# Optimization experiments

Measured on AMD Instinct MI355X. Metric: run time of the kernel, lower is better.

Reference implementation:

```python
import jax, jax.numpy as jnp
import numpy as np

VOCAB, EMB, HID, LAT, LAYERS = 32000, 512, 1024, 1024, 2
B, T = 16, 128
IN0 = EMB + HID          # layer-0 GRU input size (emb concat syn_z)
OUT_IN = HID + LAT + EMB # out-projection input (use_last_output=True)


def gru_cell(x, h, W_ih, W_hh, b_ih, b_hh):
    # PyTorch GRUCell: gates ordered [r, z, n]
    gi = x @ W_ih.T + b_ih
    gh = h @ W_hh.T + b_hh
    i_r, i_z, i_n = jnp.split(gi, 3, axis=-1)
    h_r, h_z, h_n = jnp.split(gh, 3, axis=-1)
    r = jax.nn.sigmoid(i_r + h_r)
    z = jax.nn.sigmoid(i_z + h_z)
    n = jnp.tanh(i_n + r * h_n)
    return (1.0 - z) * n + z * h


def setup_inputs() -> dict:
    key = jax.random.key(0)
    ks = jax.random.split(key, 16)
    s = 0.02
    return {
        "input_seq": jax.random.randint(ks[0], (B, T), 0, VOCAB),
        "prev_output": jnp.zeros((B, HID), jnp.float32),
        "sem_z": jax.random.normal(ks[1], (B, LAT), jnp.float32),
        "syn_z": jax.random.normal(ks[2], (B, HID), jnp.float32),
        "hidden": jnp.zeros((LAYERS, B, HID), jnp.float32),
        "emb_table": jax.random.normal(ks[3], (VOCAB, EMB), jnp.float32) * s,
        "W_ih0": jax.random.normal(ks[4], (3 * HID, IN0), jnp.float32) * s,
        "W_hh0": jax.random.normal(ks[5], (3 * HID, HID), jnp.float32) * s,
        "b_ih0": jnp.zeros((3 * HID,), jnp.float32),
        "b_hh0": jnp.zeros((3 * HID,), jnp.float32),
        "W_ih1": jax.random.normal(ks[6], (3 * HID, HID), jnp.float32) * s,
        "W_hh1": jax.random.normal(ks[7], (3 * HID, HID), jnp.float32) * s,
        "b_ih1": jnp.zeros((3 * HID,), jnp.float32),
        "b_hh1": jnp.zeros((3 * HID,), jnp.float32),
        "W_out": jax.random.normal(ks[8], (VOCAB, OUT_IN), jnp.float32) * s,
        "b_out": jnp.zeros((VOCAB,), jnp.float32),
    }


def reference(input_seq, prev_output, sem_z, syn_z, hidden, emb_table,
              W_ih0, W_hh0, b_ih0, b_hh0, W_ih1, W_hh1, b_ih1, b_hh1,
              W_out, b_out):
    # dropout=0.0 -> identity; input_feeding=False so prev_output is unused.
    embs = emb_table[input_seq]            # [B, T, E]
    embs_t = jnp.swapaxes(embs, 0, 1)      # [T, B, E]

    def step(h, emb_t):
        x = jnp.concatenate([emb_t, syn_z], axis=1)        # [B, E+H]
        h0 = gru_cell(x, h[0], W_ih0, W_hh0, b_ih0, b_hh0)  # [B, H]
        h1 = gru_cell(h0, h[1], W_ih1, W_hh1, b_ih1, b_hh1)
        pred = jnp.concatenate([h1, sem_z, emb_t], axis=1)  # [B, H+L+E]
        logits = pred @ W_out.T + b_out                     # [B, V]
        scores = jax.nn.log_softmax(logits, axis=-1)
        return jnp.stack([h0, h1]), (scores, logits)

    hidden_f, (scores, logits) = jax.lax.scan(step, hidden, embs_t)
    # scores/logits: [T, B, V]; output = last layer hidden at final step
    return scores, hidden_f, hidden_f[-1], logits
```

## Files before the change

kernel.cpp:

```cpp
#include <hip/hip_runtime.h>

typedef unsigned short u16;
typedef __attribute__((ext_vector_type(8))) short bf16x8;
typedef __attribute__((ext_vector_type(4))) float f32x4;
typedef __attribute__((ext_vector_type(4))) unsigned u32x4;

__device__ __forceinline__ float bf2f(u16 u) {
  union { unsigned u; float f; } v; v.u = ((unsigned)u) << 16; return v.f;
}
__device__ __forceinline__ u16 f2bf(float f) {
  union { float f; unsigned u; } v; v.f = f;
  unsigned r = v.u + 0x7FFFu + ((v.u >> 16) & 1u);
  return (u16)(r >> 16);
}

__device__ __forceinline__ f32x4 ld_sc_x4(const u16* p) {
  f32x4 r;
  asm volatile("global_load_dwordx4 %0, %1, off sc0 sc1"
               : "=v"(r) : "v"(p) : "memory");
  return r;
}
__device__ __forceinline__ float ld_sc_f32(const float* p) {
  float r;
  asm volatile("global_load_dword %0, %1, off sc0 sc1"
               : "=v"(r) : "v"(p) : "memory");
  return r;
}
__device__ __forceinline__ void st_sc_u16(u16* p, unsigned v) {
  asm volatile("global_store_short %0, %1, off sc0 sc1"
               :: "v"(p), "v"(v) : "memory");
}
__device__ __forceinline__ void st_sc_f32(float* p, float v) {
  asm volatile("global_store_dword %0, %1, off sc0 sc1"
               :: "v"(p), "v"(v) : "memory");
}
#define WAIT_VM0() asm volatile("s_waitcnt vmcnt(0)" ::: "memory")

constexpr size_t OFF_WCAT  = 0;
constexpr size_t OFF_WSEM  = 98304000;
constexpr size_t OFF_PART  = 98304000;
constexpr size_t OFF_H1ALL = 130000000;
constexpr size_t OFF_GI0   = 163840000;
constexpr size_t OFF_XOUT  = 189005824;
constexpr size_t OFF_H0ALL = 195297280;
constexpr size_t OFF_WIH0E = 199491584;
constexpr size_t OFF_WIH0S = 202637312;
constexpr size_t OFF_WHH0  = 208928768;
constexpr size_t OFF_WIH1  = 215220224;
constexpr size_t OFF_WHH1  = 221511680;
constexpr size_t OFF_SYNB  = 227803136;
constexpr size_t OFF_SEMB  = 228065280;
constexpr size_t OFF_BASE0 = 228327424;
constexpr size_t OFF_BASEO = 229900288;
constexpr size_t OFF_H0IBF = 246284288;
constexpr size_t OFF_H1IBF = 246317056;
constexpr size_t OFF_HIDF  = 262144000;
constexpr size_t OFF_LAST  = 262275072;
constexpr size_t OFF_LOGIT = 262340608;

__global__ __launch_bounds__(256) void conv_bf16_k(
    const float* __restrict__ src, u16* __restrict__ dst,
    int rows, int cols8, int sld, int soff, int dld, int doff) {
  int t = blockIdx.x * 256 + threadIdx.x;
  if (t >= rows * cols8) return;
  int r = t / cols8, c = (t - r * cols8) * 8;
  const float* s = src + (size_t)r * sld + soff + c;
  float4 a = *(const float4*)s;
  float4 b = *(const float4*)(s + 4);
  bf16x8 o;
  o[0] = (short)f2bf(a.x); o[1] = (short)f2bf(a.y);
  o[2] = (short)f2bf(a.z); o[3] = (short)f2bf(a.w);
  o[4] = (short)f2bf(b.x); o[5] = (short)f2bf(b.y);
  o[6] = (short)f2bf(b.z); o[7] = (short)f2bf(b.w);
  *(bf16x8*)(dst + (size_t)r * dld + doff + c) = o;
}

__global__ __launch_bounds__(256) void conv_wout_k(
    const float* __restrict__ Wout, u16* __restrict__ WCAT,
    u16* __restrict__ WSEM) {
  int t = blockIdx.x * 256 + threadIdx.x;
  int r = t / 320, c = (t - r * 320) * 8;
  const float* s = Wout + (size_t)r * 2560 + c;
  float4 a = *(const float4*)s;
  float4 b = *(const float4*)(s + 4);
  bf16x8 o;
  o[0] = (short)f2bf(a.x); o[1] = (short)f2bf(a.y);
  o[2] = (short)f2bf(a.z); o[3] = (short)f2bf(a.w);
  o[4] = (short)f2bf(b.x); o[5] = (short)f2bf(b.y);
  o[6] = (short)f2bf(b.z); o[7] = (short)f2bf(b.w);
  u16* dst;
  if (c < 1024)      dst = WCAT + (size_t)r * 1536 + c;
  else if (c < 2048) dst = WSEM + (size_t)r * 1024 + (c - 1024);
  else               dst = WCAT + (size_t)r * 1536 + 1024 + (c - 2048);
  *(bf16x8*)dst = o;
}

__global__ __launch_bounds__(256) void pack_pad_bf16_k(
    const float* __restrict__ src, u16* __restrict__ dst) {
  int t = blockIdx.x * 256 + threadIdx.x;
  int row = t >> 7, c = (t & 127) * 8;
  bf16x8 o = {0, 0, 0, 0, 0, 0, 0, 0};
  if (row < 16) {
    const float* s = src + row * 1024 + c;
    float4 a = *(const float4*)s;
    float4 b = *(const float4*)(s + 4);
    o[0] = (short)f2bf(a.x); o[1] = (short)f2bf(a.y);
    o[2] = (short)f2bf(a.z); o[3] = (short)f2bf(a.w);
    o[4] = (short)f2bf(b.x); o[5] = (short)f2bf(b.y);
    o[6] = (short)f2bf(b.z); o[7] = (short)f2bf(b.w);
  }
  *(bf16x8*)(dst + (size_t)row * 1024 + c) = o;
}

__global__ __launch_bounds__(256) void gather_emb_k(
    const int* __restrict__ seq, const float* __restrict__ table,
    u16* __restrict__ xout) {
  int t0 = blockIdx.x * 256 + threadIdx.x;
  int tb = t0 >> 6, c = (t0 & 63) * 8;
  int tt = tb >> 4, b = tb & 15;
  int tok = seq[b * 128 + tt];
  const float* s = table + (size_t)tok * 512 + c;
  float4 a = *(const float4*)s;
  float4 bb = *(const float4*)(s + 4);
  bf16x8 o;
  o[0] = (short)f2bf(a.x);  o[1] = (short)f2bf(a.y);
  o[2] = (short)f2bf(a.z);  o[3] = (short)f2bf(a.w);
  o[4] = (short)f2bf(bb.x); o[5] = (short)f2bf(bb.y);
  o[6] = (short)f2bf(bb.z); o[7] = (short)f2bf(bb.w);
  *(bf16x8*)(xout + (size_t)tb * 1536 + 1024 + c) = o;
}

__global__ __launch_bounds__(256) void init_h_k(
    const float* __restrict__ hidden, u16* __restrict__ h0b,
    u16* __restrict__ h1b) {
  int i = blockIdx.x * 256 + threadIdx.x;
  h0b[i] = f2bf(hidden[i]);
  h1b[i] = f2bf(hidden[16384 + i]);
}

__global__ __launch_bounds__(256) void sentinel_init_k(
    u32x4* __restrict__ h0, u32x4* __restrict__ h1, u32x4* __restrict__ pt) {
  int i = blockIdx.x * 256 + threadIdx.x;
  u32x4 hs = {0x7FC07FC0u, 0x7FC07FC0u, 0x7FC07FC0u, 0x7FC07FC0u};
  u32x4 ps = {0x7FC00000u, 0x7FC00000u, 0x7FC00000u, 0x7FC00000u};
  if (i < 262144) h0[i] = hs;
  else if (i < 524288) h1[i - 262144] = hs;
  else pt[i - 524288] = ps;
}

__device__ __forceinline__ void stage_tile_sent(const u16* src, char* tile,
                                                int tid, bool poll) {
  f32x4 tmp[8];
  for (;;) {
#pragma unroll
    for (int q = 0; q < 8; ++q) {
      int c = q * 256 + tid;
      int row = c >> 7, kc = c & 127;
      tmp[q] = ld_sc_x4(src + (size_t)row * 1024 + kc * 8);
    }
    WAIT_VM0();
    __builtin_amdgcn_sched_barrier(0);
    if (!poll) break;
    int bad = 0;
#pragma unroll
    for (int q = 0; q < 8; ++q) {
#pragma unroll
      for (int w = 0; w < 4; ++w) {
        unsigned x = __float_as_uint(tmp[q][w]);
        bad |= ((x & 0xFFFFu) == 0x7FC0u) | ((x >> 16) == 0x7FC0u);
      }
    }
    if (!bad) break;
    __builtin_amdgcn_s_sleep(2);
  }
#pragma unroll
  for (int q = 0; q < 8; ++q) {
    int c = q * 256 + tid;
    int row = c >> 7, kc = c & 127;
    int byte = (row * 2048 + kc * 16) ^ ((row & 7) << 4);
    *(bf16x8*)(tile + byte) = *(bf16x8*)&tmp[q];
  }
}

__global__ __launch_bounds__(256, 1) void gru_persist6_k(
    const float* __restrict__ hidden, const u16* __restrict__ h0i,
    const u16* __restrict__ h1i, const float* __restrict__ gi0,
    const u16* __restrict__ Whh0, const u16* __restrict__ Wih1,
    const u16* __restrict__ Whh1, const float* __restrict__ bhh0,
    const float* __restrict__ bih1, const float* __restrict__ bhh1,
    u16* __restrict__ h0all, u16* __restrict__ h1all, u16* __restrict__ xout,
    float* __restrict__ part, float* __restrict__ hidf,
    float* __restrict__ last) {
  extern __shared__ char ldsb[];
  char* Ab = ldsb + 98304;
  float* Cbuf = (float*)(ldsb + 131072);
  const int tid = threadIdx.x, bid = blockIdx.x;
  const int wave = tid >> 6, lane = tid & 63;
  const int role = bid >> 6, lb = bid & 63, jb = lb * 16;

  const u16* Wsrc = role == 0 ? Whh0 : (role == 1 ? Wih1 : Whh1);
  for (int idx = tid; idx < 48 * 128; idx += 256) {
    int row = idx >> 7, c = idx & 127;
    int g = row >> 4, jj2 = row & 15;
    const u16* src = Wsrc + (size_t)(g * 1024 + jb + jj2) * 1024 + c * 8;
    int byte = (row * 2048 + c * 16) ^ ((row & 7) << 4);
    *(bf16x8*)(ldsb + byte) = *(const bf16x8*)src;
  }

  const int eb = tid >> 4, jj = tid & 15, j = jb + jj;
  float hp = 0.f, bR = 0.f, bZ = 0.f, bN = 0.f, iR = 0.f, iZ = 0.f, iN = 0.f;
  if (role == 0) {
    hp = hidden[eb * 1024 + j];
    bR = bhh0[j]; bZ = bhh0[1024 + j]; bN = bhh0[2048 + j];
  } else if (role == 2) {
    hp = hidden[16384 + eb * 1024 + j];
    bR = bhh1[j]; bZ = bhh1[1024 + j]; bN = bhh1[2048 + j];
    iR = bih1[j]; iZ = bih1[1024 + j]; iN = bih1[2048 + j];
  }
  __syncthreads();

  const int arow = lane & 15, aq = lane >> 4;
  for (int t = 0; t < 128; ++t) {
    float* Cl = Cbuf + (t & 1) * 3456;
    const u16* asrc;
    bool poll;
    if (role == 0)      { asrc = t ? h0all + (size_t)(t - 1) * 16384 : h0i; poll = t > 0; }
    else if (role == 1) { asrc = h0all + (size_t)t * 16384; poll = true; }
    else                { asrc = t ? h1all + (size_t)(t - 1) * 16384 : h1i; poll = t > 0; }
    stage_tile_sent(asrc, Ab, tid, poll);
    __syncthreads();

    {
      f32x4 a0 = {0.f, 0.f, 0.f, 0.f}, a1 = a0, a2 = a0;
#pragma unroll
      for (int i = 0; i < 8; ++i) {
        int ks = wave + i * 4;
        int abyte = (arow * 2048 + ks * 64 + aq * 16) ^ ((arow & 7) << 4);
        bf16x8 af = *(const bf16x8*)(Ab + abyte);
        int r0 = arow, r1 = 16 + arow, r2 = 32 + arow;
        bf16x8 b0 = *(const bf16x8*)(
            ldsb + ((r0 * 2048 + ks * 64 + aq * 16) ^ ((r0 & 7) << 4)));
        bf16x8 b1 = *(const bf16x8*)(
            ldsb + ((r1 * 2048 + ks * 64 + aq * 16) ^ ((r1 & 7) << 4)));
        bf16x8 b2 = *(const bf16x8*)(
            ldsb + ((r2 * 2048 + ks * 64 + aq * 16) ^ ((r2 & 7) << 4)));
        a0 = __builtin_amdgcn_mfma_f32_16x16x32_bf16(af, b0, a0, 0, 0, 0);
        a1 = __builtin_amdgcn_mfma_f32_16x16x32_bf16(af, b1, a1, 0, 0, 0);
        a2 = __builtin_amdgcn_mfma_f32_16x16x32_bf16(af, b2, a2, 0, 0, 0);
      }
#pragma unroll
      for (int r = 0; r < 4; ++r) {
        int ci = (aq * 4 + r) * 16 + arow + aq * 8;
        Cl[(0 * 4 + wave) * 288 + ci] = a0[r];
        Cl[(1 * 4 + wave) * 288 + ci] = a1[r];
        Cl[(2 * 4 + wave) * 288 + ci] = a2[r];
      }
    }
    __syncthreads();

    {
      int ci = eb * 16 + jj + (eb >> 2) * 8;
      float s0 = Cl[0 * 288 + ci] + Cl[1 * 288 + ci] +
                 Cl[2 * 288 + ci] + Cl[3 * 288 + ci];
      float s1 = Cl[4 * 288 + ci] + Cl[5 * 288 + ci] +
                 Cl[6 * 288 + ci] + Cl[7 * 288 + ci];
      float s2 = Cl[8 * 288 + ci] + Cl[9 * 288 + ci] +
                 Cl[10 * 288 + ci] + Cl[11 * 288 + ci];
      if (role == 1) {
        float* pp = part + ((size_t)t * 64 + lb) * 768 + eb * 16 + jj;
        st_sc_f32(pp, s0);
        st_sc_f32(pp + 256, s1);
        st_sc_f32(pp + 512, s2);
        WAIT_VM0();
      } else {
        float ir, iz, inn;
        if (role == 0) {
          const float* g = gi0 + ((size_t)t * 16 + eb) * 3072 + j;
          ir = g[0]; iz = g[1024]; inn = g[2048];
        } else {
          const float* pp = part + ((size_t)t * 64 + lb) * 768 + eb * 16 + jj;
          float p0, p1, p2;
          for (;;) {
            p0 = ld_sc_f32(pp); p1 = ld_sc_f32(pp + 256);
            p2 = ld_sc_f32(pp + 512);
            WAIT_VM0();
            __builtin_amdgcn_sched_barrier(0);
            int bad = (__float_as_uint(p0) == 0x7FC00000u) |
                      (__float_as_uint(p1) == 0x7FC00000u) |
                      (__float_as_uint(p2) == 0x7FC00000u);
            if (!bad) break;
            __builtin_amdgcn_s_sleep(2);
          }
          ir = p0 + iR; iz = p1 + iZ; inn = p2 + iN;
        }
        float r = 1.f / (1.f + __expf(-(ir + s0 + bR)));
        float z = 1.f / (1.f + __expf(-(iz + s1 + bZ)));
        float n = tanhf(inn + r * (s2 + bN));
        float hnew = (1.f - z) * n + z * hp;
        hp = hnew;
        u16 hb = f2bf(hnew);
        if (role == 0) {
          st_sc_u16(h0all + ((size_t)t * 16 + eb) * 1024 + j, (unsigned)hb);
          if (t == 127) hidf[eb * 1024 + j] = hnew;
        } else {
          st_sc_u16(h1all + ((size_t)t * 16 + eb) * 1024 + j, (unsigned)hb);
          xout[((size_t)t * 16 + eb) * 1536 + j] = hb;
          if (t == 127) {
            hidf[16384 + eb * 1024 + j] = hnew;
            last[eb * 1024 + j] = hnew;
          }
        }
        WAIT_VM0();
      }
    }
  }
}

template <int MODE>
__global__ __launch_bounds__(256) void gemm_bt_k(
    const u16* __restrict__ A, int lda, const u16* __restrict__ Bw, int ldb,
    float* __restrict__ C, int ldc, const float* __restrict__ add,
    int N, int K) {
  __shared__ u16 Asm_[128 * 32];
  __shared__ u16 Bsm_[128 * 32];
  const int m0 = blockIdx.x * 128, n0 = blockIdx.y * 128;
  const int tid = threadIdx.x, wave = tid >> 6, lane = tid & 63;
  const int wm = (wave >> 1) * 64, wn = (wave & 1) * 64;
  const int lrow = lane & 15, lk = (lane >> 4) * 8;
  f32x4 acc[4][4] = {};
  for (int k0 = 0; k0 < K; k0 += 32) {
    __syncthreads();
#pragma unroll
    for (int q = 0; q < 2; ++q) {
      int c = (wave * 2 + q) * 64 + lane;
      int row = c >> 2, seg = c & 3;
      const u16* src = A + (size_t)(m0 + row) * lda + k0 + seg * 8;
      u16* dst = Asm_ + (wave * 2 + q) * 512;
      __builtin_amdgcn_global_load_lds(
          (const __attribute__((address_space(1))) void*)src,
          (__attribute__((address_space(3))) void*)dst, 16, 0, 0);
    }
#pragma unroll
    for (int q = 0; q < 2; ++q) {
      int c = (wave * 2 + q) * 64 + lane;
      int row = c >> 2, seg = c & 3;
      const u16* src = Bw + (size_t)(n0 + row) * ldb + k0 + seg * 8;
      u16* dst = Bsm_ + (wave * 2 + q) * 512;
      __builtin_amdgcn_global_load_lds(
          (const __attribute__((address_space(1))) void*)src,
          (__attribute__((address_space(3))) void*)dst, 16, 0, 0);
    }
    asm volatile("s_waitcnt vmcnt(0)" ::: "memory");
    __syncthreads();
    bf16x8 af[4], bfr[4];
#pragma unroll
    for (int i = 0; i < 4; ++i) {
      af[i]  = *(const bf16x8*)(Asm_ + (wm + i * 16 + lrow) * 32 + lk);
      bfr[i] = *(const bf16x8*)(Bsm_ + (wn + i * 16 + lrow) * 32 + lk);
    }
#pragma unroll
    for (int i = 0; i < 4; ++i)
#pragma unroll
      for (int jx = 0; jx < 4; ++jx)
        acc[i][jx] = __builtin_amdgcn_mfma_f32_16x16x32_bf16(
            af[i], bfr[jx], acc[i][jx], 0, 0, 0);
  }
  const int lr4 = (lane >> 4) * 4;
#pragma unroll
  for (int i = 0; i < 4; ++i) {
#pragma unroll
    for (int jx = 0; jx < 4; ++jx) {
      int gc = n0 + wn + jx * 16 + lrow;
#pragma unroll
      for (int r = 0; r < 4; ++r) {
        int gr = m0 + wm + i * 16 + lr4 + r;
        float v = acc[i][jx][r];
        if (MODE == 1) v += add[(gr & 15) * N + gc];
        else if (MODE == 2) v += add[gc];
        C[(size_t)gr * ldc + gc] = v;
      }
    }
  }
}

template <int MODE, bool SWZ>
__global__ __launch_bounds__(512) void gemm256_bt_k(
    const u16* __restrict__ A, int lda, const u16* __restrict__ Bw, int ldb,
    float* __restrict__ C, int ldc, const float* __restrict__ add,
    int N, int K) {
  __shared__ u16 Asm_[256 * 32];
  __shared__ u16 Bsm_[128 * 32];
  int bx = blockIdx.x, by = blockIdx.y;
  if (SWZ) {
    int nx = gridDim.x;
    int orig = by * nx + bx;
    int cpx = (nx * gridDim.y) >> 3;
    int wg = (orig & 7) * cpx + (orig >> 3);
    bx = wg % nx; by = wg / nx;
  }
  const int m0 = bx * 256, n0 = by * 128;
  const int tid = threadIdx.x, wave = tid >> 6, lane = tid & 63;
  const int wm = (wave >> 1) * 64, wn = (wave & 1) * 64;
  const int lrow = lane & 15, lk = (lane >> 4) * 8;
  f32x4 acc[4][4] = {};
  for (int k0 = 0; k0 < K; k0 += 32) {
    __syncthreads();
#pragma unroll
    for (int q = 0; q < 2; ++q) {
      int c = (q * 8 + wave) * 64 + lane;
      int row = c >> 2, seg = c & 3;
      const u16* src = A + (size_t)(m0 + row) * lda + k0 + seg * 8;
      u16* dst = Asm_ + (q * 8 + wave) * 512;
      __builtin_amdgcn_global_load_lds(
          (const __attribute__((address_space(1))) void*)src,
          (__attribute__((address_space(3))) void*)dst, 16, 0, 0);
    }
    {
      int c = wave * 64 + lane;
      int row = c >> 2, seg = c & 3;
      const u16* src = Bw + (size_t)(n0 + row) * ldb + k0 + seg * 8;
      u16* dst = Bsm_ + wave * 512;
      __builtin_amdgcn_global_load_lds(
          (const __attribute__((address_space(1))) void*)src,
          (__attribute__((address_space(3))) void*)dst, 16, 0, 0);
    }
    asm volatile("s_waitcnt vmcnt(0)" ::: "memory");
    __syncthreads();
    bf16x8 af[4], bfr[4];
#pragma unroll
    for (int i = 0; i < 4; ++i) {
      af[i]  = *(const bf16x8*)(Asm_ + (wm + i * 16 + lrow) * 32 + lk);
      bfr[i] = *(const bf16x8*)(Bsm_ + (wn + i * 16 + lrow) * 32 + lk);
    }
#pragma unroll
    for (int i = 0; i < 4; ++i)
#pragma unroll
      for (int jx = 0; jx < 4; ++jx)
        acc[i][jx] = __builtin_amdgcn_mfma_f32_16x16x32_bf16(
            af[i], bfr[jx], acc[i][jx], 0, 0, 0);
  }
  const int lr4 = (lane >> 4) * 4;
#pragma unroll
  for (int i = 0; i < 4; ++i) {
#pragma unroll
    for (int jx = 0; jx < 4; ++jx) {
      int gc = n0 + wn + jx * 16 + lrow;
#pragma unroll
      for (int r = 0; r < 4; ++r) {
        int gr = m0 + wm + i * 16 + lr4 + r;
        float v = acc[i][jx][r];
        if (MODE == 1) v += add[(gr & 15) * N + gc];
        else if (MODE == 2) v += add[gc];
        C[(size_t)gr * ldc + gc] = v;
      }
    }
  }
}

__global__ __launch_bounds__(256) void log_softmax_k(
    const float* __restrict__ logits, float* __restrict__ scores) {
  int row = blockIdx.x;
  const float* x = logits + (size_t)row * 32000;
  float* y = scores + (size_t)row * 32000;
  __shared__ float redm[4], reds[4];
  int tid = threadIdx.x;
  float m = -3.4e38f, s = 0.f;
  for (int idx = tid * 4; idx < 32000; idx += 1024) {
    float4 v = *(const float4*)(x + idx);
    float cm = fmaxf(fmaxf(v.x, v.y), fmaxf(v.z, v.w));
    if (cm > m) { s *= __expf(m - cm); m = cm; }
    s += __expf(v.x - m) + __expf(v.y - m) + __expf(v.z - m) + __expf(v.w - m);
  }
  for (int off = 1; off < 64; off <<= 1) {
    float mo = __shfl_xor(m, off), so = __shfl_xor(s, off);
    float nm = fmaxf(m, mo);
    s = s * __expf(m - nm) + so * __expf(mo - nm);
    m = nm;
  }
  if ((tid & 63) == 0) { redm[tid >> 6] = m; reds[tid >> 6] = s; }
  __syncthreads();
  {
    float fm = fmaxf(fmaxf(redm[0], redm[1]), fmaxf(redm[2], redm[3]));
    float fs = reds[0] * __expf(redm[0] - fm) + reds[1] * __expf(redm[1] - fm) +
               reds[2] * __expf(redm[2] - fm) + reds[3] * __expf(redm[3] - fm);
    float lse = fm + logf(fs);
    for (int idx = tid * 4; idx < 32000; idx += 1024) {
      float4 v = *(const float4*)(x + idx);
      float4 o;
      o.x = v.x - lse; o.y = v.y - lse; o.z = v.z - lse; o.w = v.w - lse;
      *(float4*)(y + idx) = o;
    }
  }
}

extern "C" void kernel_launch(void* const* d_in, const int* in_sizes, int n_in,
                              void* d_out, int out_size, void* d_ws,
                              size_t ws_size, hipStream_t stream) {
  const int*   seq    = (const int*)d_in[0];
  const float* sem    = (const float*)d_in[2];
  const float* syn    = (const float*)d_in[3];
  const float* hidden = (const float*)d_in[4];
  const float* table  = (const float*)d_in[5];
  const float* Wih0   = (const float*)d_in[6];
  const float* Whh0   = (const float*)d_in[7];
  const float* bih0   = (const float*)d_in[8];
  const float* bhh0   = (const float*)d_in[9];
  const float* Wih1   = (const float*)d_in[10];
  const float* Whh1   = (const float*)d_in[11];
  const float* bih1   = (const float*)d_in[12];
  const float* bhh1   = (const float*)d_in[13];
  const float* Wout   = (const float*)d_in[14];
  const float* bout   = (const float*)d_in[15];

  char* base = (char*)d_out;
  float* scores = (float*)base;
  u16*   WCAT   = (u16*)(base + OFF_WCAT);
  u16*   WSEM   = (u16*)(base + OFF_WSEM);
  float* PART   = (float*)(base + OFF_PART);
  u16*   H1ALL  = (u16*)(base + OFF_H1ALL);
  float* GI0    = (float*)(base + OFF_GI0);
  u16*   XOUT   = (u16*)(base + OFF_XOUT);
  u16*   H0ALL  = (u16*)(base + OFF_H0ALL);
  u16*   WIH0E  = (u16*)(base + OFF_WIH0E);
  u16*   WIH0S  = (u16*)(base + OFF_WIH0S);
  u16*   WHH0B  = (u16*)(base + OFF_WHH0);
  u16*   WIH1B  = (u16*)(base + OFF_WIH1);
  u16*   WHH1B  = (u16*)(base + OFF_WHH1);
  u16*   SYNB   = (u16*)(base + OFF_SYNB);
  u16*   SEMB   = (u16*)(base + OFF_SEMB);
  float* BASE0  = (float*)(base + OFF_BASE0);
  float* BASEO  = (float*)(base + OFF_BASEO);
  u16*   H0IBF  = (u16*)(base + OFF_H0IBF);
  u16*   H1IBF  = (u16*)(base + OFF_H1IBF);
  float* hidf   = (float*)(base + OFF_HIDF);
  float* last   = (float*)(base + OFF_LAST);
  float* logits = (float*)(base + OFF_LOGIT);

  conv_wout_k<<<40000, 256, 0, stream>>>(Wout, WCAT, WSEM);
  conv_bf16_k<<<768, 256, 0, stream>>>(Wih0, WIH0E, 3072, 64, 1536, 0, 512, 0);
  conv_bf16_k<<<1536, 256, 0, stream>>>(Wih0, WIH0S, 3072, 128, 1536, 512, 1024, 0);
  conv_bf16_k<<<1536, 256, 0, stream>>>(Whh0, WHH0B, 3072, 128, 1024, 0, 1024, 0);
  conv_bf16_k<<<1536, 256, 0, stream>>>(Wih1, WIH1B, 3072, 128, 1024, 0, 1024, 0);
  conv_bf16_k<<<1536, 256, 0, stream>>>(Whh1, WHH1B, 3072, 128, 1024, 0, 1024, 0);

  gather_emb_k<<<512, 256, 0, stream>>>(seq, table, XOUT);
  pack_pad_bf16_k<<<64, 256, 0, stream>>>(syn, SYNB);
  pack_pad_bf16_k<<<64, 256, 0, stream>>>(sem, SEMB);
  init_h_k<<<64, 256, 0, stream>>>(hidden, H0IBF, H1IBF);

  gemm_bt_k<2><<<dim3(1, 24), 256, 0, stream>>>(
      SYNB, 1024, WIH0S, 1024, BASE0, 3072, bih0, 3072, 1024);
  gemm_bt_k<2><<<dim3(1, 250), 256, 0, stream>>>(
      SEMB, 1024, WSEM, 1024, BASEO, 32000, bout, 32000, 1024);

  gemm256_bt_k<1, true><<<dim3(8, 24), 512, 0, stream>>>(
      XOUT + 1024, 1536, WIH0E, 512, GI0, 3072, BASE0, 3072, 512);

  sentinel_init_k<<<8192, 256, 0, stream>>>(
      (u32x4*)H0ALL, (u32x4*)H1ALL, (u32x4*)PART);

  hipFuncSetAttribute((const void*)gru_persist6_k,
                      hipFuncAttributeMaxDynamicSharedMemorySize, 158720);
  gru_persist6_k<<<192, 256, 158720, stream>>>(
      hidden, H0IBF, H1IBF, GI0, WHH0B, WIH1B, WHH1B, bhh0, bih1, bhh1,
      H0ALL, H1ALL, XOUT, PART, hidf, last);

  gemm256_bt_k<1, true><<<dim3(8, 250), 512, 0, stream>>>(
      XOUT, 1536, WCAT, 1536, logits, 32000, BASEO, 32000, 1536);

  log_softmax_k<<<2048, 256, 0, stream>>>(logits, scores);
}
```

Baseline: 1.270 ms.

## Replace sentinel polling with flag sync and overlap Wout prep inside GRU kernel

```diff
diff --git a/kernel.cpp b/kernel.cpp
--- a/kernel.cpp
+++ b/kernel.cpp
@@ -3,7 +3,6 @@
 typedef unsigned short u16;
 typedef __attribute__((ext_vector_type(8))) short bf16x8;
 typedef __attribute__((ext_vector_type(4))) float f32x4;
-typedef __attribute__((ext_vector_type(4))) unsigned u32x4;
 
 __device__ __forceinline__ float bf2f(u16 u) {
   union { unsigned u; float f; } v; v.u = ((unsigned)u) << 16; return v.f;
@@ -36,8 +35,14 @@
 }
 #define WAIT_VM0() asm volatile("s_waitcnt vmcnt(0)" ::: "memory")
 
+__device__ __forceinline__ int ld_flag(const int* p) {
+  return __hip_atomic_load(p, __ATOMIC_RELAXED, __HIP_MEMORY_SCOPE_AGENT);
+}
+__device__ __forceinline__ void st_flag(int* p, int v) {
+  __hip_atomic_store(p, v, __ATOMIC_RELAXED, __HIP_MEMORY_SCOPE_AGENT);
+}
+
 constexpr size_t OFF_WCAT  = 0;
-constexpr size_t OFF_WSEM  = 98304000;
 constexpr size_t OFF_PART  = 98304000;
 constexpr size_t OFF_H1ALL = 130000000;
 constexpr size_t OFF_GI0   = 163840000;
@@ -49,11 +54,11 @@
 constexpr size_t OFF_WIH1  = 215220224;
 constexpr size_t OFF_WHH1  = 221511680;
 constexpr size_t OFF_SYNB  = 227803136;
-constexpr size_t OFF_SEMB  = 228065280;
 constexpr size_t OFF_BASE0 = 228327424;
 constexpr size_t OFF_BASEO = 229900288;
 constexpr size_t OFF_H0IBF = 246284288;
 constexpr size_t OFF_H1IBF = 246317056;
+constexpr size_t OFF_FLAGS = 246349824;
 constexpr size_t OFF_HIDF  = 262144000;
 constexpr size_t OFF_LAST  = 262275072;
 constexpr size_t OFF_LOGIT = 262340608;
@@ -73,26 +78,6 @@
   o[4] = (short)f2bf(b.x); o[5] = (short)f2bf(b.y);
   o[6] = (short)f2bf(b.z); o[7] = (short)f2bf(b.w);
   *(bf16x8*)(dst + (size_t)r * dld + doff + c) = o;
-}
-
-__global__ __launch_bounds__(256) void conv_wout_k(
-    const float* __restrict__ Wout, u16* __restrict__ WCAT,
-    u16* __restrict__ WSEM) {
-  int t = blockIdx.x * 256 + threadIdx.x;
-  int r = t / 320, c = (t - r * 320) * 8;
-  const float* s = Wout + (size_t)r * 2560 + c;
-  float4 a = *(const float4*)s;
-  float4 b = *(const float4*)(s + 4);
-  bf16x8 o;
-  o[0] = (short)f2bf(a.x); o[1] = (short)f2bf(a.y);
-  o[2] = (short)f2bf(a.z); o[3] = (short)f2bf(a.w);
-  o[4] = (short)f2bf(b.x); o[5] = (short)f2bf(b.y);
-  o[6] = (short)f2bf(b.z); o[7] = (short)f2bf(b.w);
-  u16* dst;
-  if (c < 1024)      dst = WCAT + (size_t)r * 1536 + c;
-  else if (c < 2048) dst = WSEM + (size_t)r * 1024 + (c - 1024);
-  else               dst = WCAT + (size_t)r * 1536 + 1024 + (c - 2048);
-  *(bf16x8*)dst = o;
 }
 
 __global__ __launch_bounds__(256) void pack_pad_bf16_k(
@@ -132,47 +117,28 @@
 
 __global__ __launch_bounds__(256) void init_h_k(
     const float* __restrict__ hidden, u16* __restrict__ h0b,
-    u16* __restrict__ h1b) {
+    u16* __restrict__ h1b, int* __restrict__ flags) {
   int i = blockIdx.x * 256 + threadIdx.x;
   h0b[i] = f2bf(hidden[i]);
   h1b[i] = f2bf(hidden[16384 + i]);
-}
-
-__global__ __launch_bounds__(256) void sentinel_init_k(
-    u32x4* __restrict__ h0, u32x4* __restrict__ h1, u32x4* __restrict__ pt) {
-  int i = blockIdx.x * 256 + threadIdx.x;
-  u32x4 hs = {0x7FC07FC0u, 0x7FC07FC0u, 0x7FC07FC0u, 0x7FC07FC0u};
-  u32x4 ps = {0x7FC00000u, 0x7FC00000u, 0x7FC00000u, 0x7FC00000u};
-  if (i < 262144) h0[i] = hs;
-  else if (i < 524288) h1[i - 262144] = hs;
-  else pt[i - 524288] = ps;
-}
-
-__device__ __forceinline__ void stage_tile_sent(const u16* src, char* tile,
-                                                int tid, bool poll) {
+  if (i < 4096) flags[i] = 0;
+}
+
+__device__ __forceinline__ void stage_tile_flag(
+    const u16* src, char* tile, int tid, const int* fl, int target) {
+  if (fl) {
+    const int* myf = fl + ((tid & 127) >> 1) * 16;
+    while (ld_flag(myf) < target) __builtin_amdgcn_s_sleep(1);
+  }
   f32x4 tmp[8];
-  for (;;) {
-#pragma unroll
-    for (int q = 0; q < 8; ++q) {
-      int c = q * 256 + tid;
-      int row = c >> 7, kc = c & 127;
-      tmp[q] = ld_sc_x4(src + (size_t)row * 1024 + kc * 8);
-    }
-    WAIT_VM0();
-    __builtin_amdgcn_sched_barrier(0);
-    if (!poll) break;
-    int bad = 0;
-#pragma unroll
-    for (int q = 0; q < 8; ++q) {
-#pragma unroll
-      for (int w = 0; w < 4; ++w) {
-        unsigned x = __float_as_uint(tmp[q][w]);
-        bad |= ((x & 0xFFFFu) == 0x7FC0u) | ((x >> 16) == 0x7FC0u);
-      }
-    }
-    if (!bad) break;
-    __builtin_amdgcn_s_sleep(2);
-  }
+#pragma unroll
+  for (int q = 0; q < 8; ++q) {
+    int c = q * 256 + tid;
+    int row = c >> 7, kc = c & 127;
+    tmp[q] = ld_sc_x4(src + (size_t)row * 1024 + kc * 8);
+  }
+  WAIT_VM0();
+  __builtin_amdgcn_sched_barrier(0);
 #pragma unroll
   for (int q = 0; q < 8; ++q) {
     int c = q * 256 + tid;
@@ -182,7 +148,7 @@
   }
 }
 
-__global__ __launch_bounds__(256, 1) void gru_persist6_k(
+__global__ __launch_bounds__(256, 1) void gru_persist7_k(
     const float* __restrict__ hidden, const u16* __restrict__ h0i,
     const u16* __restrict__ h1i, const float* __restrict__ gi0,
     const u16* __restrict__ Whh0, const u16* __restrict__ Wih1,
@@ -190,13 +156,68 @@
     const float* __restrict__ bih1, const float* __restrict__ bhh1,
     u16* __restrict__ h0all, u16* __restrict__ h1all, u16* __restrict__ xout,
     float* __restrict__ part, float* __restrict__ hidf,
-    float* __restrict__ last) {
+    float* __restrict__ last, int* __restrict__ flags,
+    const float* __restrict__ Wout, const float* __restrict__ bout,
+    const float* __restrict__ sem, u16* __restrict__ WCAT,
+    float* __restrict__ baseo) {
   extern __shared__ char ldsb[];
+  const int tid = threadIdx.x, bid = blockIdx.x;
+  const int wave = tid >> 6, lane = tid & 63;
+
+  if (bid >= 192) {
+    const int ab = bid - 192;
+    float* semLds = (float*)ldsb;
+    for (int i = tid; i < 16384; i += 256) {
+      int b = i >> 10, k = i & 1023;
+      semLds[b * 1025 + k] = sem[i];
+    }
+    __syncthreads();
+    {
+      const int b = lane & 15, kq = lane >> 4;
+      for (int r = ab * 4 + wave; r < 32000; r += 256) {
+        const float* w = Wout + (size_t)r * 2560 + 1024 + kq * 256;
+        const float* sv = semLds + b * 1025 + kq * 256;
+        float a0 = 0.f, a1 = 0.f, a2 = 0.f, a3 = 0.f;
+#pragma unroll 4
+        for (int k = 0; k < 256; k += 16) {
+          float4 w0 = *(const float4*)(w + k);
+          float4 w1 = *(const float4*)(w + k + 4);
+          float4 w2 = *(const float4*)(w + k + 8);
+          float4 w3 = *(const float4*)(w + k + 12);
+          a0 += w0.x * sv[k] + w0.y * sv[k + 1] + w0.z * sv[k + 2] + w0.w * sv[k + 3];
+          a1 += w1.x * sv[k + 4] + w1.y * sv[k + 5] + w1.z * sv[k + 6] + w1.w * sv[k + 7];
+          a2 += w2.x * sv[k + 8] + w2.y * sv[k + 9] + w2.z * sv[k + 10] + w2.w * sv[k + 11];
+          a3 += w3.x * sv[k + 12] + w3.y * sv[k + 13] + w3.z * sv[k + 14] + w3.w * sv[k + 15];
+        }
+        float v = (a0 + a1) + (a2 + a3);
+        v += __shfl_xor(v, 16);
+        v += __shfl_xor(v, 32);
+        if (lane < 16) baseo[b * 32000 + r] = v + bout[r];
+      }
+    }
+    for (int job = ab * 256 + tid; job < 32000 * 192; job += 64 * 256) {
+      int r = job / 192, c = job - r * 192;
+      int scol = c < 128 ? c * 8 : 2048 + (c - 128) * 8;
+      int dcol = c < 128 ? c * 8 : 1024 + (c - 128) * 8;
+      const float* s = Wout + (size_t)r * 2560 + scol;
+      float4 a = *(const float4*)s;
+      float4 b = *(const float4*)(s + 4);
+      bf16x8 o;
+      o[0] = (short)f2bf(a.x); o[1] = (short)f2bf(a.y);
+      o[2] = (short)f2bf(a.z); o[3] = (short)f2bf(a.w);
+      o[4] = (short)f2bf(b.x); o[5] = (short)f2bf(b.y);
+      o[6] = (short)f2bf(b.z); o[7] = (short)f2bf(b.w);
+      *(bf16x8*)(WCAT + (size_t)r * 1536 + dcol) = o;
+    }
+    return;
+  }
+
   char* Ab = ldsb + 98304;
   float* Cbuf = (float*)(ldsb + 131072);
-  const int tid = threadIdx.x, bid = blockIdx.x;
-  const int wave = tid >> 6, lane = tid & 63;
   const int role = bid >> 6, lb = bid & 63, jb = lb * 16;
+  int* f0 = flags;
+  int* fih = flags + 1024;
+  int* f1 = flags + 2048;
 
   const u16* Wsrc = role == 0 ? Whh0 : (role == 1 ? Wih1 : Whh1);
   for (int idx = tid; idx < 48 * 128; idx += 256) {
@@ -223,11 +244,19 @@
   for (int t = 0; t < 128; ++t) {
     float* Cl = Cbuf + (t & 1) * 3456;
     const u16* asrc;
-    bool poll;
-    if (role == 0)      { asrc = t ? h0all + (size_t)(t - 1) * 16384 : h0i; poll = t > 0; }
-    else if (role == 1) { asrc = h0all + (size_t)t * 16384; poll = true; }
-    else                { asrc = t ? h1all + (size_t)(t - 1) * 16384 : h1i; poll = t > 0; }
-    stage_tile_sent(asrc, Ab, tid, poll);
+    const int* fl;
+    int target;
+    if (role == 0) {
+      asrc = t ? h0all + (size_t)(t - 1) * 16384 : h0i;
+      fl = t ? f0 : nullptr; target = t;
+    } else if (role == 1) {
+      asrc = h0all + (size_t)t * 16384;
+      fl = f0; target = t + 1;
+    } else {
+      asrc = t ? h1all + (size_t)(t - 1) * 16384 : h1i;
+      fl = t ? f1 : nullptr; target = t;
+    }
+    stage_tile_flag(asrc, Ab, tid, fl, target);
     __syncthreads();
 
     {
@@ -256,6 +285,8 @@
         Cl[(2 * 4 + wave) * 288 + ci] = a2[r];
       }
     }
+    if (role == 2 && tid == 0)
+      while (ld_flag(fih + lb * 16) < t + 1) __builtin_amdgcn_s_sleep(1);
     __syncthreads();
 
     {
@@ -279,18 +310,10 @@
           ir = g[0]; iz = g[1024]; inn = g[2048];
         } else {
           const float* pp = part + ((size_t)t * 64 + lb) * 768 + eb * 16 + jj;
-          float p0, p1, p2;
-          for (;;) {
-            p0 = ld_sc_f32(pp); p1 = ld_sc_f32(pp + 256);
-            p2 = ld_sc_f32(pp + 512);
-            WAIT_VM0();
-            __builtin_amdgcn_sched_barrier(0);
-            int bad = (__float_as_uint(p0) == 0x7FC00000u) |
-                      (__float_as_uint(p1) == 0x7FC00000u) |
-                      (__float_as_uint(p2) == 0x7FC00000u);
-            if (!bad) break;
-            __builtin_amdgcn_s_sleep(2);
-          }
+          float p0 = ld_sc_f32(pp), p1 = ld_sc_f32(pp + 256),
+                p2 = ld_sc_f32(pp + 512);
+          WAIT_VM0();
+          __builtin_amdgcn_sched_barrier(0);
           ir = p0 + iR; iz = p1 + iZ; inn = p2 + iN;
         }
         float r = 1.f / (1.f + __expf(-(ir + s0 + bR)));
@@ -313,6 +336,12 @@
         WAIT_VM0();
       }
     }
+    __syncthreads();
+    if (tid == 0) {
+      if (role == 0)      st_flag(f0 + lb * 16, t + 1);
+      else if (role == 1) st_flag(fih + lb * 16, t + 1);
+      else                st_flag(f1 + lb * 16, t + 1);
+    }
   }
 }
 
@@ -515,7 +544,6 @@
   char* base = (char*)d_out;
   float* scores = (float*)base;
   u16*   WCAT   = (u16*)(base + OFF_WCAT);
-  u16*   WSEM   = (u16*)(base + OFF_WSEM);
   float* PART   = (float*)(base + OFF_PART);
   u16*   H1ALL  = (u16*)(base + OFF_H1ALL);
   float* GI0    = (float*)(base + OFF_GI0);
@@ -527,16 +555,15 @@
   u16*   WIH1B  = (u16*)(base + OFF_WIH1);
   u16*   WHH1B  = (u16*)(base + OFF_WHH1);
   u16*   SYNB   = (u16*)(base + OFF_SYNB);
-  u16*   SEMB   = (u16*)(base + OFF_SEMB);
   float* BASE0  = (float*)(base + OFF_BASE0);
   float* BASEO  = (float*)(base + OFF_BASEO);
   u16*   H0IBF  = (u16*)(base + OFF_H0IBF);
   u16*   H1IBF  = (u16*)(base + OFF_H1IBF);
+  int*   FLAGS  = (int*)(base + OFF_FLAGS);
   float* hidf   = (float*)(base + OFF_HIDF);
   float* last   = (float*)(base + OFF_LAST);
   float* logits = (float*)(base + OFF_LOGIT);
 
-  conv_wout_k<<<40000, 256, 0, stream>>>(Wout, WCAT, WSEM);
   conv_bf16_k<<<768, 256, 0, stream>>>(Wih0, WIH0E, 3072, 64, 1536, 0, 512, 0);
   conv_bf16_k<<<1536, 256, 0, stream>>>(Wih0, WIH0S, 3072, 128, 1536, 512, 1024, 0);
   conv_bf16_k<<<1536, 256, 0, stream>>>(Whh0, WHH0B, 3072, 128, 1024, 0, 1024, 0);
@@ -545,25 +572,20 @@
 
   gather_emb_k<<<512, 256, 0, stream>>>(seq, table, XOUT);
   pack_pad_bf16_k<<<64, 256, 0, stream>>>(syn, SYNB);
-  pack_pad_bf16_k<<<64, 256, 0, stream>>>(sem, SEMB);
-  init_h_k<<<64, 256, 0, stream>>>(hidden, H0IBF, H1IBF);
+  init_h_k<<<64, 256, 0, stream>>>(hidden, H0IBF, H1IBF, FLAGS);
 
   gemm_bt_k<2><<<dim3(1, 24), 256, 0, stream>>>(
       SYNB, 1024, WIH0S, 1024, BASE0, 3072, bih0, 3072, 1024);
-  gemm_bt_k<2><<<dim3(1, 250), 256, 0, stream>>>(
-      SEMB, 1024, WSEM, 1024, BASEO, 32000, bout, 32000, 1024);
 
   gemm256_bt_k<1, true><<<dim3(8, 24), 512, 0, stream>>>(
       XOUT + 1024, 1536, WIH0E, 512, GI0, 3072, BASE0, 3072, 512);
 
-  sentinel_init_k<<<8192, 256, 0, stream>>>(
-      (u32x4*)H0ALL, (u32x4*)H1ALL, (u32x4*)PART);
-
-  hipFuncSetAttribute((const void*)gru_persist6_k,
+  hipFuncSetAttribute((const void*)gru_persist7_k,
                       hipFuncAttributeMaxDynamicSharedMemorySize, 158720);
-  gru_persist6_k<<<192, 256, 158720, stream>>>(
+  gru_persist7_k<<<256, 256, 158720, stream>>>(
       hidden, H0IBF, H1IBF, GI0, WHH0B, WIH1B, WHH1B, bhh0, bih1, bhh1,
-      H0ALL, H1ALL, XOUT, PART, hidf, last);
+      H0ALL, H1ALL, XOUT, PART, hidf, last, FLAGS,
+      Wout, bout, sem, WCAT, BASEO);
 
   gemm256_bt_k<1, true><<<dim3(8, 250), 512, 0, stream>>>(
       XOUT, 1536, WCAT, 1536, logits, 32000, BASEO, 32000, 1536);
```

Measured after the change: 1.470 ms. 1.16x slower.

## Replace NaN-sentinel polling with per-block progress flags in persistent GRU

Applied to the files above, without the earlier changes.

```diff
diff --git a/kernel.cpp b/kernel.cpp
--- a/kernel.cpp
+++ b/kernel.cpp
@@ -3,7 +3,6 @@
 typedef unsigned short u16;
 typedef __attribute__((ext_vector_type(8))) short bf16x8;
 typedef __attribute__((ext_vector_type(4))) float f32x4;
-typedef __attribute__((ext_vector_type(4))) unsigned u32x4;
 
 __device__ __forceinline__ float bf2f(u16 u) {
   union { unsigned u; float f; } v; v.u = ((unsigned)u) << 16; return v.f;
@@ -35,6 +34,13 @@
                :: "v"(p), "v"(v) : "memory");
 }
 #define WAIT_VM0() asm volatile("s_waitcnt vmcnt(0)" ::: "memory")
+
+__device__ __forceinline__ int ld_flag(const int* p) {
+  return __hip_atomic_load(p, __ATOMIC_RELAXED, __HIP_MEMORY_SCOPE_AGENT);
+}
+__device__ __forceinline__ void st_flag(int* p, int v) {
+  __hip_atomic_store(p, v, __ATOMIC_RELAXED, __HIP_MEMORY_SCOPE_AGENT);
+}
 
 constexpr size_t OFF_WCAT  = 0;
 constexpr size_t OFF_WSEM  = 98304000;
@@ -54,6 +60,7 @@
 constexpr size_t OFF_BASEO = 229900288;
 constexpr size_t OFF_H0IBF = 246284288;
 constexpr size_t OFF_H1IBF = 246317056;
+constexpr size_t OFF_FLAGS = 246349824;
 constexpr size_t OFF_HIDF  = 262144000;
 constexpr size_t OFF_LAST  = 262275072;
 constexpr size_t OFF_LOGIT = 262340608;
@@ -132,47 +139,24 @@
 
 __global__ __launch_bounds__(256) void init_h_k(
     const float* __restrict__ hidden, u16* __restrict__ h0b,
-    u16* __restrict__ h1b) {
+    u16* __restrict__ h1b, int* __restrict__ flags) {
   int i = blockIdx.x * 256 + threadIdx.x;
   h0b[i] = f2bf(hidden[i]);
   h1b[i] = f2bf(hidden[16384 + i]);
-}
-
-__global__ __launch_bounds__(256) void sentinel_init_k(
-    u32x4* __restrict__ h0, u32x4* __restrict__ h1, u32x4* __restrict__ pt) {
-  int i = blockIdx.x * 256 + threadIdx.x;
-  u32x4 hs = {0x7FC07FC0u, 0x7FC07FC0u, 0x7FC07FC0u, 0x7FC07FC0u};
-  u32x4 ps = {0x7FC00000u, 0x7FC00000u, 0x7FC00000u, 0x7FC00000u};
-  if (i < 262144) h0[i] = hs;
-  else if (i < 524288) h1[i - 262144] = hs;
-  else pt[i - 524288] = ps;
-}
-
-__device__ __forceinline__ void stage_tile_sent(const u16* src, char* tile,
-                                                int tid, bool poll) {
+  if (i < 4096) flags[i] = 0;
+}
+
+__device__ __forceinline__ void stage_tile(const u16* src, char* tile,
+                                           int tid) {
   f32x4 tmp[8];
-  for (;;) {
-#pragma unroll
-    for (int q = 0; q < 8; ++q) {
-      int c = q * 256 + tid;
-      int row = c >> 7, kc = c & 127;
-      tmp[q] = ld_sc_x4(src + (size_t)row * 1024 + kc * 8);
-    }
-    WAIT_VM0();
-    __builtin_amdgcn_sched_barrier(0);
-    if (!poll) break;
-    int bad = 0;
-#pragma unroll
-    for (int q = 0; q < 8; ++q) {
-#pragma unroll
-      for (int w = 0; w < 4; ++w) {
-        unsigned x = __float_as_uint(tmp[q][w]);
-        bad |= ((x & 0xFFFFu) == 0x7FC0u) | ((x >> 16) == 0x7FC0u);
-      }
-    }
-    if (!bad) break;
-    __builtin_amdgcn_s_sleep(2);
-  }
+#pragma unroll
+  for (int q = 0; q < 8; ++q) {
+    int c = q * 256 + tid;
+    int row = c >> 7, kc = c & 127;
+    tmp[q] = ld_sc_x4(src + (size_t)row * 1024 + kc * 8);
+  }
+  WAIT_VM0();
+  __builtin_amdgcn_sched_barrier(0);
 #pragma unroll
   for (int q = 0; q < 8; ++q) {
     int c = q * 256 + tid;
@@ -182,7 +166,7 @@
   }
 }
 
-__global__ __launch_bounds__(256, 1) void gru_persist6_k(
+__global__ __launch_bounds__(256, 1) void gru_persist3_k(
     const float* __restrict__ hidden, const u16* __restrict__ h0i,
     const u16* __restrict__ h1i, const float* __restrict__ gi0,
     const u16* __restrict__ Whh0, const u16* __restrict__ Wih1,
@@ -190,13 +174,14 @@
     const float* __restrict__ bih1, const float* __restrict__ bhh1,
     u16* __restrict__ h0all, u16* __restrict__ h1all, u16* __restrict__ xout,
     float* __restrict__ part, float* __restrict__ hidf,
-    float* __restrict__ last) {
+    float* __restrict__ last, int* __restrict__ flags) {
   extern __shared__ char ldsb[];
   char* Ab = ldsb + 98304;
-  float* Cbuf = (float*)(ldsb + 131072);
+  float* Cl = (float*)(ldsb + 131072);
   const int tid = threadIdx.x, bid = blockIdx.x;
   const int wave = tid >> 6, lane = tid & 63;
   const int role = bid >> 6, lb = bid & 63, jb = lb * 16;
+  int* f0 = flags, *fih = flags + 1024, *f1 = flags + 2048;
 
   const u16* Wsrc = role == 0 ? Whh0 : (role == 1 ? Wih1 : Whh1);
   for (int idx = tid; idx < 48 * 128; idx += 256) {
@@ -221,13 +206,23 @@
 
   const int arow = lane & 15, aq = lane >> 4;
   for (int t = 0; t < 128; ++t) {
-    float* Cl = Cbuf + (t & 1) * 3456;
+    if (role == 0) {
+      if (t > 0 && tid < 64)
+        while (ld_flag(f0 + tid * 16) < t) __builtin_amdgcn_s_sleep(1);
+    } else if (role == 1) {
+      if (tid < 64)
+        while (ld_flag(f0 + tid * 16) < t + 1) __builtin_amdgcn_s_sleep(1);
+    } else {
+      if (t > 0 && tid < 64)
+        while (ld_flag(f1 + tid * 16) < t) __builtin_amdgcn_s_sleep(1);
+    }
+    __syncthreads();
+
     const u16* asrc;
-    bool poll;
-    if (role == 0)      { asrc = t ? h0all + (size_t)(t - 1) * 16384 : h0i; poll = t > 0; }
-    else if (role == 1) { asrc = h0all + (size_t)t * 16384; poll = true; }
-    else                { asrc = t ? h1all + (size_t)(t - 1) * 16384 : h1i; poll = t > 0; }
-    stage_tile_sent(asrc, Ab, tid, poll);
+    if (role == 0)      asrc = t ? h0all + (size_t)(t - 1) * 16384 : h0i;
+    else if (role == 1) asrc = h0all + (size_t)t * 16384;
+    else                asrc = t ? h1all + (size_t)(t - 1) * 16384 : h1i;
+    stage_tile(asrc, Ab, tid);
     __syncthreads();
 
     {
@@ -256,6 +251,8 @@
         Cl[(2 * 4 + wave) * 288 + ci] = a2[r];
       }
     }
+    if (role == 2 && tid == 0)
+      while (ld_flag(fih + lb * 16) < t + 1) __builtin_amdgcn_s_sleep(1);
     __syncthreads();
 
     {
@@ -279,18 +276,10 @@
           ir = g[0]; iz = g[1024]; inn = g[2048];
         } else {
           const float* pp = part + ((size_t)t * 64 + lb) * 768 + eb * 16 + jj;
-          float p0, p1, p2;
-          for (;;) {
-            p0 = ld_sc_f32(pp); p1 = ld_sc_f32(pp + 256);
-            p2 = ld_sc_f32(pp + 512);
-            WAIT_VM0();
-            __builtin_amdgcn_sched_barrier(0);
-            int bad = (__float_as_uint(p0) == 0x7FC00000u) |
-                      (__float_as_uint(p1) == 0x7FC00000u) |
-                      (__float_as_uint(p2) == 0x7FC00000u);
-            if (!bad) break;
-            __builtin_amdgcn_s_sleep(2);
-          }
+          float p0 = ld_sc_f32(pp), p1 = ld_sc_f32(pp + 256),
+                p2 = ld_sc_f32(pp + 512);
+          WAIT_VM0();
+          __builtin_amdgcn_sched_barrier(0);
           ir = p0 + iR; iz = p1 + iZ; inn = p2 + iN;
         }
         float r = 1.f / (1.f + __expf(-(ir + s0 + bR)));
@@ -313,6 +302,12 @@
         WAIT_VM0();
       }
     }
+    __syncthreads();
+    if (tid == 0) {
+      if (role == 0)      st_flag(f0 + lb * 16, t + 1);
+      else if (role == 1) st_flag(fih + lb * 16, t + 1);
+      else                st_flag(f1 + lb * 16, t + 1);
+    }
   }
 }
 
@@ -532,6 +527,7 @@
   float* BASEO  = (float*)(base + OFF_BASEO);
   u16*   H0IBF  = (u16*)(base + OFF_H0IBF);
   u16*   H1IBF  = (u16*)(base + OFF_H1IBF);
+  int*   FLAGS  = (int*)(base + OFF_FLAGS);
   float* hidf   = (float*)(base + OFF_HIDF);
   float* last   = (float*)(base + OFF_LAST);
   float* logits = (float*)(base + OFF_LOGIT);
@@ -546,7 +542,7 @@
   gather_emb_k<<<512, 256, 0, stream>>>(seq, table, XOUT);
   pack_pad_bf16_k<<<64, 256, 0, stream>>>(syn, SYNB);
   pack_pad_bf16_k<<<64, 256, 0, stream>>>(sem, SEMB);
-  init_h_k<<<64, 256, 0, stream>>>(hidden, H0IBF, H1IBF);
+  init_h_k<<<64, 256, 0, stream>>>(hidden, H0IBF, H1IBF, FLAGS);
 
   gemm_bt_k<2><<<dim3(1, 24), 256, 0, stream>>>(
       SYNB, 1024, WIH0S, 1024, BASE0, 3072, bih0, 3072, 1024);
@@ -556,14 +552,11 @@
   gemm256_bt_k<1, true><<<dim3(8, 24), 512, 0, stream>>>(
       XOUT + 1024, 1536, WIH0E, 512, GI0, 3072, BASE0, 3072, 512);
 
-  sentinel_init_k<<<8192, 256, 0, stream>>>(
-      (u32x4*)H0ALL, (u32x4*)H1ALL, (u32x4*)PART);
-
-  hipFuncSetAttribute((const void*)gru_persist6_k,
-                      hipFuncAttributeMaxDynamicSharedMemorySize, 158720);
-  gru_persist6_k<<<192, 256, 158720, stream>>>(
+  hipFuncSetAttribute((const void*)gru_persist3_k,
+                      hipFuncAttributeMaxDynamicSharedMemorySize, 145408);
+  gru_persist3_k<<<192, 256, 145408, stream>>>(
       hidden, H0IBF, H1IBF, GI0, WHH0B, WIH1B, WHH1B, bhh0, bih1, bhh1,
-      H0ALL, H1ALL, XOUT, PART, hidf, last);
+      H0ALL, H1ALL, XOUT, PART, hidf, last, FLAGS);
 
   gemm256_bt_k<1, true><<<dim3(8, 250), 512, 0, stream>>>(
       XOUT, 1536, WCAT, 1536, logits, 32000, BASEO, 32000, 1536);
```

After: 1.136 ms. 10.6% less time.
